# Optimization experiments

Measured on AMD Instinct MI355X. Metric: run time of the kernel, lower is better.

## Reference

```python
import jax, jax.numpy as jnp
import numpy as np

B, N, KNB, F, H = 1, 50000, 16, 128, 128
BN_EPS = 1e-3  # keras BatchNormalization default epsilon
ALPHA = 0.3    # keras LeakyReLU default negative slope


def setup_inputs() -> dict:
    key = jax.random.key(0)
    ks = jax.random.split(key, 14)
    s_in = 1.0 / np.sqrt(F)
    s_cat = 1.0 / np.sqrt(F + H)
    return {
        'embeddings': jax.random.normal(ks[0], (B, N, F), jnp.float32),
        'weights': jnp.zeros((1, 1), jnp.float32),  # unused in call_att
        'neighbor_set': jax.random.randint(ks[1], (B, N, KNB), 0, N),
        'Wq': jax.random.normal(ks[2], (F, H), jnp.float32) * s_in,
        'bq': jnp.zeros((H,), jnp.float32),
        'Wk': jax.random.normal(ks[3], (F, H), jnp.float32) * s_in,
        'bk': jnp.zeros((H,), jnp.float32),
        'Wv': jax.random.normal(ks[4], (F, H), jnp.float32) * s_in,
        'bv': jnp.zeros((H,), jnp.float32),
        'W1': jax.random.normal(ks[5], (F + H, H), jnp.float32) * s_cat,
        'b1': jnp.zeros((H,), jnp.float32),
        'gamma': 1.0 + 0.1 * jax.random.normal(ks[6], (H,), jnp.float32),
        'beta': 0.1 * jax.random.normal(ks[7], (H,), jnp.float32),
        'mov_mean': 0.1 * jax.random.normal(ks[8], (H,), jnp.float32),
        'mov_var': 1.0 + 0.1 * jax.random.uniform(ks[9], (H,), jnp.float32),
    }


def reference(embeddings, weights, neighbor_set, Wq, bq, Wk, bk, Wv, bv,
              W1, b1, gamma, beta, mov_mean, mov_var):
    lrelu = lambda x: jax.nn.leaky_relu(x, ALPHA)
    # batched gather: nb[b, n, k] = embeddings[b, neighbor_set[b, n, k]]  -> [B,N,K,F]
    nb = jax.vmap(lambda e, idx: e[idx])(embeddings, neighbor_set)
    q = lrelu(embeddings @ Wq + bq)      # [B,N,H]
    k = lrelu(nb @ Wk + bk)              # [B,N,K,H]
    v = lrelu(nb @ Wv + bv)              # [B,N,K,H]
    # Q is tiled across the K neighbor rows in the original; every attention row
    # is identical, so mean-pool over rows == single-query attention. Same math.
    scores = jnp.einsum('bnh,bnkh->bnk', q, k)          # dot-product, no scale
    attn = jax.nn.softmax(scores, axis=-1)
    pooled = jnp.einsum('bnk,bnkh->bnh', attn, v)       # [B,N,H]
    h = lrelu(jnp.concatenate([embeddings, pooled], axis=-1) @ W1 + b1)
    h = h / (jnp.linalg.norm(h, axis=2, keepdims=True) + 1e-6)
    # BatchNormalization (inference form, axis=-1)
    return gamma * (h - mov_mean) * jax.lax.rsqrt(mov_var + BN_EPS) + beta
```

## Files before the change

### kernel.cpp

```cpp
#include <hip/hip_runtime.h>
#include <hip/hip_bf16.h>

#define N_NODES 50000
#define KNB 16
#define FDIM 128
#define HDIM 128
#define ALPHA 0.3f
#define BN_EPS 1e-3f

typedef __bf16 v8bf __attribute__((ext_vector_type(8)));
typedef float v4f __attribute__((ext_vector_type(4)));
typedef unsigned short ushort_t;

__device__ __forceinline__ float blo(unsigned int u) {
    union { float f; unsigned int i; } x; x.i = u << 16; return x.f;
}
__device__ __forceinline__ float bhi(unsigned int u) {
    union { float f; unsigned int i; } x; x.i = u & 0xffff0000u; return x.f;
}

__device__ __forceinline__ unsigned short f2bf(float f) {
    union { float f; unsigned int u; } x;
    x.f = f;
    unsigned int r = x.u + 0x7fffu + ((x.u >> 16) & 1u);
    return (unsigned short)(r >> 16);
}

__device__ __forceinline__ unsigned int pk2(float a, float b) {
    __hip_bfloat162 h = __float22bfloat162_rn(make_float2(a, b));
    union { __hip_bfloat162 h; unsigned int u; } r; r.h = h; return r.u;
}

__device__ __forceinline__ float lrelu(float x) { return x > 0.f ? x : ALPHA * x; }

__device__ __forceinline__ v8bf load8f(const float* p) {
    float4 A = ((const float4*)p)[0];
    float4 B = ((const float4*)p)[1];
    union { v8bf v; unsigned int u[4]; } r;
    r.u[0] = pk2(A.x, A.y); r.u[1] = pk2(A.z, A.w);
    r.u[2] = pk2(B.x, B.y); r.u[3] = pk2(B.z, B.w);
    return r.v;
}

__global__ __launch_bounds__(256) void prep_kernel(
    const float* __restrict__ Wq, const float* __restrict__ Wk,
    const float* __restrict__ Wv, const float* __restrict__ W1,
    ushort_t* __restrict__ WT)
{
    const int idx = blockIdx.x * 256 + threadIdx.x;
    if (idx < 16384) {
        int k = idx >> 7, n = idx & 127;
        WT[n * 128 + k] = f2bf(Wq[idx]);
    } else if (idx < 32768) {
        int i = idx - 16384; int k = i >> 7, n = i & 127;
        WT[16384 + n * 128 + k] = f2bf(Wk[i]);
    } else if (idx < 49152) {
        int i = idx - 32768; int k = i >> 7, n = i & 127;
        WT[32768 + n * 128 + k] = f2bf(Wv[i]);
    } else if (idx < 81920) {
        int i = idx - 49152; int k = i >> 7, n = i & 127;
        WT[49152 + n * 256 + k] = f2bf(W1[i]);
    }
}

#define QSTRIDE 560
#define KVSTRIDE 528
#define WTILE 18432

__global__ __launch_bounds__(256) void qkv_kernel(
    const float* __restrict__ E, const ushort_t* __restrict__ WT,
    const float* __restrict__ bq, const float* __restrict__ bk,
    const float* __restrict__ bv,
    float* __restrict__ Qo, ushort_t* __restrict__ KV)
{
    __shared__ char smem[4 * WTILE];

    const int tid  = threadIdx.x;
    const int wave = tid >> 6;
    const int lane = tid & 63;
    const int quad = lane >> 4;
    const int j    = lane & 15;
    const int row0 = blockIdx.x * 128 + wave * 32;

    char* const wbase = smem + wave * WTILE;

    const int ar0 = min(row0 + j,      N_NODES - 1);
    const int ar1 = min(row0 + 16 + j, N_NODES - 1);

    v8bf a0f[4], a1f[4];
#pragma unroll
    for (int ks = 0; ks < 4; ++ks) {
        const int k0 = ks * 32 + quad * 8;
        a0f[ks] = load8f(E + (size_t)ar0 * FDIM + k0);
        a1f[ks] = load8f(E + (size_t)ar1 * FDIM + k0);
    }

    const float* biases[3] = {bq, bk, bv};

    for (int w = 0; w < 3; ++w) {
        const ushort_t* __restrict__ Wsrc = WT + w * 16384;

        v4f acc[2][8];
#pragma unroll
        for (int rb = 0; rb < 2; ++rb)
#pragma unroll
            for (int c = 0; c < 8; ++c) acc[rb][c] = (v4f){0.f, 0.f, 0.f, 0.f};

#pragma unroll
        for (int ks = 0; ks < 4; ++ks) {
            const int k0 = ks * 32 + quad * 8;
            v8bf b[8];
#pragma unroll
            for (int c = 0; c < 8; ++c)
                b[c] = *(const v8bf*)(Wsrc + (c * 16 + j) * 128 + k0);
#pragma unroll
            for (int c = 0; c < 8; ++c) {
                acc[0][c] = __builtin_amdgcn_mfma_f32_16x16x32_bf16(b[c], a0f[ks], acc[0][c], 0, 0, 0);
                acc[1][c] = __builtin_amdgcn_mfma_f32_16x16x32_bf16(b[c], a1f[ks], acc[1][c], 0, 0, 0);
            }
        }

        const float* __restrict__ bias = biases[w];

        if (w == 0) {
#pragma unroll
            for (int rb = 0; rb < 2; ++rb)
#pragma unroll
                for (int c = 0; c < 8; ++c) {
                    const float4 bb = ((const float4*)bias)[c * 4 + quad];
                    v4f v = acc[rb][c];
                    v[0] = lrelu(v[0] + bb.x); v[1] = lrelu(v[1] + bb.y);
                    v[2] = lrelu(v[2] + bb.z); v[3] = lrelu(v[3] + bb.w);
                    *(v4f*)(wbase + (rb * 16 + j) * QSTRIDE + (c * 16 + quad * 4) * 4) = v;
                }
#pragma unroll
            for (int t = 0; t < 16; ++t) {
                const int r  = 2 * t + (lane >> 5);
                const v4f v  = *(const v4f*)(wbase + r * QSTRIDE + (lane & 31) * 16);
                const int gr = row0 + r;
                if (gr < N_NODES)
                    *(v4f*)(Qo + (size_t)gr * HDIM + (lane & 31) * 4) = v;
            }
        } else {
            const int voff = (w == 2) ? 256 : 0;
#pragma unroll
            for (int rb = 0; rb < 2; ++rb)
#pragma unroll
                for (int c = 0; c < 8; ++c) {
                    const float4 bb = ((const float4*)bias)[c * 4 + quad];
                    const v4f v = acc[rb][c];
                    uint2 u;
                    u.x = pk2(lrelu(v[0] + bb.x), lrelu(v[1] + bb.y));
                    u.y = pk2(lrelu(v[2] + bb.z), lrelu(v[3] + bb.w));
                    *(uint2*)(wbase + (rb * 16 + j) * KVSTRIDE + (c * 16 + quad * 4) * 2 + voff) = u;
                }
            if (w == 2) {
#pragma unroll
                for (int t = 0; t < 16; ++t) {
                    const int r  = 2 * t + (lane >> 5);
                    const uint4 v = *(const uint4*)(wbase + r * KVSTRIDE + (lane & 31) * 16);
                    const int gr = row0 + r;
                    if (gr < N_NODES)
                        *(uint4*)((char*)KV + (size_t)gr * 512 + (lane & 31) * 16) = v;
                }
            }
        }
    }
}

#define DOT8(qa, qb, kp) (qa.x*blo(kp.x) + qa.y*bhi(kp.x) + qa.z*blo(kp.y) + qa.w*bhi(kp.y) \
                        + qb.x*blo(kp.z) + qb.y*bhi(kp.z) + qb.z*blo(kp.w) + qb.w*bhi(kp.w))

__global__ __launch_bounds__(256) void attn_kernel(
    float* __restrict__ QP, const ushort_t* __restrict__ KV,
    const int* __restrict__ nbr)
{
    const int tid  = threadIdx.x;
    const int wave = tid >> 6;
    const int lane = tid & 63;
    const int grp  = lane >> 4;
    const int li   = lane & 15;
    const int n0 = __builtin_amdgcn_readfirstlane(blockIdx.x * 8 + wave * 2);
    const int n1 = n0 + 1;

    const float4* qr0 = (const float4*)(QP + (size_t)n0 * HDIM + li * 8);
    const float4 q0a = qr0[0], q0b = qr0[1];
    const float4* qr1 = (const float4*)(QP + (size_t)n1 * HDIM + li * 8);
    const float4 q1a = qr1[0], q1b = qr1[1];

    const int* nbA = nbr + n0 * KNB;
    const int* nbB = nbr + n1 * KNB;
    int nidA[4], nidB[4];
#pragma unroll
    for (int t = 0; t < 4; ++t) {
        int a0 = nbA[t*4+0]; a0 = ((unsigned)a0 < (unsigned)N_NODES) ? a0 : 0;
        int a1 = nbA[t*4+1]; a1 = ((unsigned)a1 < (unsigned)N_NODES) ? a1 : 0;
        int a2 = nbA[t*4+2]; a2 = ((unsigned)a2 < (unsigned)N_NODES) ? a2 : 0;
        int a3 = nbA[t*4+3]; a3 = ((unsigned)a3 < (unsigned)N_NODES) ? a3 : 0;
        int va = a0;
        va = (grp == 1) ? a1 : va;
        va = (grp == 2) ? a2 : va;
        va = (grp == 3) ? a3 : va;
        nidA[t] = va;
        int b0 = nbB[t*4+0]; b0 = ((unsigned)b0 < (unsigned)N_NODES) ? b0 : 0;
        int b1 = nbB[t*4+1]; b1 = ((unsigned)b1 < (unsigned)N_NODES) ? b1 : 0;
        int b2 = nbB[t*4+2]; b2 = ((unsigned)b2 < (unsigned)N_NODES) ? b2 : 0;
        int b3 = nbB[t*4+3]; b3 = ((unsigned)b3 < (unsigned)N_NODES) ? b3 : 0;
        int vb = b0;
        vb = (grp == 1) ? b1 : vb;
        vb = (grp == 2) ? b2 : vb;
        vb = (grp == 3) ? b3 : vb;
        nidB[t] = vb;
    }

    const char* kvb = (const char*)KV;
    const size_t lo16 = (size_t)(li * 16);

    uint4 kA[4], kB[4], vA[4], vB[4];
#pragma unroll
    for (int t = 0; t < 4; ++t) {
        kA[t] = *(const uint4*)(kvb + (size_t)nidA[t] * 512 + lo16);
        kB[t] = *(const uint4*)(kvb + (size_t)nidB[t] * 512 + lo16);
        vA[t] = *(const uint4*)(kvb + (size_t)nidA[t] * 512 + 256 + lo16);
        vB[t] = *(const uint4*)(kvb + (size_t)nidB[t] * 512 + 256 + lo16);
    }

    float sA[4], sB[4];
#pragma unroll
    for (int t = 0; t < 4; ++t) {
        sA[t] = DOT8(q0a, q0b, kA[t]);
        sB[t] = DOT8(q1a, q1b, kB[t]);
    }
#pragma unroll
    for (int off = 1; off <= 8; off <<= 1) {
#pragma unroll
        for (int t = 0; t < 4; ++t) {
            sA[t] += __shfl_xor(sA[t], off, 64);
            sB[t] += __shfl_xor(sB[t], off, 64);
        }
    }

    float mA = fmaxf(fmaxf(sA[0], sA[1]), fmaxf(sA[2], sA[3]));
    float mB = fmaxf(fmaxf(sB[0], sB[1]), fmaxf(sB[2], sB[3]));
    mA = fmaxf(mA, __shfl_xor(mA, 16, 64)); mB = fmaxf(mB, __shfl_xor(mB, 16, 64));
    mA = fmaxf(mA, __shfl_xor(mA, 32, 64)); mB = fmaxf(mB, __shfl_xor(mB, 32, 64));
    float aA[4], aB[4];
#pragma unroll
    for (int t = 0; t < 4; ++t) {
        aA[t] = __expf(sA[t] - mA);
        aB[t] = __expf(sB[t] - mB);
    }
    float sumA = aA[0] + aA[1] + aA[2] + aA[3];
    float sumB = aB[0] + aB[1] + aB[2] + aB[3];
    sumA += __shfl_xor(sumA, 16, 64); sumB += __shfl_xor(sumB, 16, 64);
    sumA += __shfl_xor(sumA, 32, 64); sumB += __shfl_xor(sumB, 32, 64);
    const float invA = 1.f / sumA, invB = 1.f / sumB;
#pragma unroll
    for (int t = 0; t < 4; ++t) { aA[t] *= invA; aB[t] *= invB; }

    float pA[8] = {0,0,0,0,0,0,0,0}, pB[8] = {0,0,0,0,0,0,0,0};
#pragma unroll
    for (int t = 0; t < 4; ++t) {
        pA[0] += aA[t] * blo(vA[t].x); pA[1] += aA[t] * bhi(vA[t].x);
        pA[2] += aA[t] * blo(vA[t].y); pA[3] += aA[t] * bhi(vA[t].y);
        pA[4] += aA[t] * blo(vA[t].z); pA[5] += aA[t] * bhi(vA[t].z);
        pA[6] += aA[t] * blo(vA[t].w); pA[7] += aA[t] * bhi(vA[t].w);
        pB[0] += aB[t] * blo(vB[t].x); pB[1] += aB[t] * bhi(vB[t].x);
        pB[2] += aB[t] * blo(vB[t].y); pB[3] += aB[t] * bhi(vB[t].y);
        pB[4] += aB[t] * blo(vB[t].z); pB[5] += aB[t] * bhi(vB[t].z);
        pB[6] += aB[t] * blo(vB[t].w); pB[7] += aB[t] * bhi(vB[t].w);
    }
#pragma unroll
    for (int i = 0; i < 8; ++i) {
        pA[i] += __shfl_xor(pA[i], 16, 64); pB[i] += __shfl_xor(pB[i], 16, 64);
        pA[i] += __shfl_xor(pA[i], 32, 64); pB[i] += __shfl_xor(pB[i], 32, 64);
    }

    if (grp == 0) {
        float4* out = (float4*)(QP + (size_t)n0 * HDIM + li * 8);
        out[0] = make_float4(pA[0], pA[1], pA[2], pA[3]);
        out[1] = make_float4(pA[4], pA[5], pA[6], pA[7]);
    } else if (grp == 1) {
        float4* out = (float4*)(QP + (size_t)n1 * HDIM + li * 8);
        out[0] = make_float4(pB[0], pB[1], pB[2], pB[3]);
        out[1] = make_float4(pB[4], pB[5], pB[6], pB[7]);
    }
}

__global__ __launch_bounds__(256) void out_kernel(
    const float* __restrict__ E, const ushort_t* __restrict__ W1T,
    const float* __restrict__ b1,
    const float* __restrict__ gamma, const float* __restrict__ beta,
    const float* __restrict__ mmean, const float* __restrict__ mvar,
    float* __restrict__ OutP)
{
    __shared__ ushort_t sW[128 * 136];

    const int tid  = threadIdx.x;
    const int wave = tid >> 6;
    const int lane = tid & 63;
    const int quad = lane >> 4;
    const int j    = lane & 15;
    const int row0 = blockIdx.x * 128 + wave * 32;

    const int ar0 = min(row0 + j,      N_NODES - 1);
    const int ar1 = min(row0 + 16 + j, N_NODES - 1);

    v4f acc[2][8];
#pragma unroll
    for (int rb = 0; rb < 2; ++rb)
#pragma unroll
        for (int c = 0; c < 8; ++c) acc[rb][c] = (v4f){0.f, 0.f, 0.f, 0.f};

    for (int half = 0; half < 2; ++half) {
        for (int i = tid; i < 2048; i += 256) {
            int n = i >> 4, kc = i & 15;
            *(uint4*)(&sW[n * 136 + kc * 8]) =
                *(const uint4*)(W1T + n * 256 + half * 128 + kc * 8);
        }
        __syncthreads();

        const float* Abase = (half == 0) ? E : (const float*)OutP;
#pragma unroll
        for (int ks = 0; ks < 4; ++ks) {
            const int k0 = ks * 32 + quad * 8;
            v8bf a0 = load8f(Abase + (size_t)ar0 * 128 + k0);
            v8bf a1 = load8f(Abase + (size_t)ar1 * 128 + k0);
            v8bf b[8];
#pragma unroll
            for (int c = 0; c < 8; ++c)
                b[c] = *(const v8bf*)(&sW[(c * 16 + j) * 136 + k0]);
#pragma unroll
            for (int c = 0; c < 8; ++c) {
                acc[0][c] = __builtin_amdgcn_mfma_f32_16x16x32_bf16(a0, b[c], acc[0][c], 0, 0, 0);
                acc[1][c] = __builtin_amdgcn_mfma_f32_16x16x32_bf16(a1, b[c], acc[1][c], 0, 0, 0);
            }
        }
        __syncthreads();
    }

    float scale_[8], shift_[8], bias_[8];
#pragma unroll
    for (int c = 0; c < 8; ++c) {
        const int col = c * 16 + j;
        const float sc = gamma[col] * rsqrtf(mvar[col] + BN_EPS);
        scale_[c] = sc;
        shift_[c] = beta[col] - mmean[col] * sc;
        bias_[c]  = b1[col];
    }

#pragma unroll
    for (int rb = 0; rb < 2; ++rb)
#pragma unroll
        for (int c = 0; c < 8; ++c)
#pragma unroll
            for (int i = 0; i < 4; ++i)
                acc[rb][c][i] = lrelu(acc[rb][c][i] + bias_[c]);

#pragma unroll
    for (int rb = 0; rb < 2; ++rb) {
#pragma unroll
        for (int i = 0; i < 4; ++i) {
            float ss = 0.f;
#pragma unroll
            for (int c = 0; c < 8; ++c) ss += acc[rb][c][i] * acc[rb][c][i];
            ss += __shfl_xor(ss, 1, 64);
            ss += __shfl_xor(ss, 2, 64);
            ss += __shfl_xor(ss, 4, 64);
            ss += __shfl_xor(ss, 8, 64);
            const float invn = 1.f / (sqrtf(ss) + 1e-6f);
            const int r = row0 + rb * 16 + quad * 4 + i;
            if (r < N_NODES) {
#pragma unroll
                for (int c = 0; c < 8; ++c)
                    OutP[(size_t)r * HDIM + c * 16 + j] =
                        acc[rb][c][i] * invn * scale_[c] + shift_[c];
            }
        }
    }
}

extern "C" void kernel_launch(void* const* d_in, const int* in_sizes, int n_in,
                              void* d_out, int out_size, void* d_ws, size_t ws_size,
                              hipStream_t stream)
{
    const float* E     = (const float*)d_in[0];
    const int*   nbr   = (const int*)d_in[2];
    const float* Wq    = (const float*)d_in[3];
    const float* bq    = (const float*)d_in[4];
    const float* Wk    = (const float*)d_in[5];
    const float* bk    = (const float*)d_in[6];
    const float* Wv    = (const float*)d_in[7];
    const float* bv    = (const float*)d_in[8];
    const float* W1    = (const float*)d_in[9];
    const float* b1    = (const float*)d_in[10];
    const float* gam   = (const float*)d_in[11];
    const float* bet   = (const float*)d_in[12];
    const float* mmean = (const float*)d_in[13];
    const float* mvar  = (const float*)d_in[14];

    ushort_t* KV = (ushort_t*)d_ws;
    ushort_t* WT = KV + (size_t)N_NODES * 256;
    float* QP = (float*)d_out;

    const int gridA = (N_NODES + 127) / 128;
    prep_kernel<<<320, 256, 0, stream>>>(Wq, Wk, Wv, W1, WT);
    qkv_kernel<<<gridA, 256, 0, stream>>>(E, WT, bq, bk, bv, QP, KV);
    attn_kernel<<<N_NODES / 8, 256, 0, stream>>>(QP, KV, nbr);
    out_kernel<<<gridA, 256, 0, stream>>>(E, WT + 49152, b1, gam, bet, mmean, mvar, QP);
}
```

Before: 211.6 us.

## Fuse attention and output GEMM into one launch with per-block ready flags

Merges the attention and output kernels into a single grid: the first blocks do attention and set per-block flags after writing pooled rows, and the later blocks compute the E-half of the output GEMM, then spin on flags before reading pooled rows through atomic (cache-bypassing) loads. This is meant to remove a kernel launch boundary and overlap the E·W1 half with the attention tail. It relies on blocks being dispatched in index order to avoid deadlock. It adds spin-wait and atomic load/store overhead.

```diff
diff --git a/kernel.cpp b/kernel.cpp
--- a/kernel.cpp
+++ b/kernel.cpp
@@ -7,6 +7,8 @@
 #define HDIM 128
 #define ALPHA 0.3f
 #define BN_EPS 1e-3f
+#define NATT 6250
+#define NOUT 391
 
 typedef __bf16 v8bf __attribute__((ext_vector_type(8)));
 typedef float v4f __attribute__((ext_vector_type(4)));
@@ -42,10 +44,29 @@
     return r.v;
 }
 
+__device__ __forceinline__ void st8_bypass(float* p, float a, float b) {
+    union { float f[2]; unsigned long long u; } x;
+    x.f[0] = a; x.f[1] = b;
+    __hip_atomic_store((unsigned long long*)p, x.u, __ATOMIC_RELAXED,
+                       __HIP_MEMORY_SCOPE_AGENT);
+}
+__device__ __forceinline__ v8bf load8f_bypass(const float* p) {
+    union { unsigned long long u; float f[2]; } d0, d1, d2, d3;
+    const unsigned long long* q = (const unsigned long long*)p;
+    d0.u = __hip_atomic_load(q + 0, __ATOMIC_RELAXED, __HIP_MEMORY_SCOPE_AGENT);
+    d1.u = __hip_atomic_load(q + 1, __ATOMIC_RELAXED, __HIP_MEMORY_SCOPE_AGENT);
+    d2.u = __hip_atomic_load(q + 2, __ATOMIC_RELAXED, __HIP_MEMORY_SCOPE_AGENT);
+    d3.u = __hip_atomic_load(q + 3, __ATOMIC_RELAXED, __HIP_MEMORY_SCOPE_AGENT);
+    union { v8bf v; unsigned int u[4]; } r;
+    r.u[0] = pk2(d0.f[0], d0.f[1]); r.u[1] = pk2(d1.f[0], d1.f[1]);
+    r.u[2] = pk2(d2.f[0], d2.f[1]); r.u[3] = pk2(d3.f[0], d3.f[1]);
+    return r.v;
+}
+
 __global__ __launch_bounds__(256) void prep_kernel(
     const float* __restrict__ Wq, const float* __restrict__ Wk,
     const float* __restrict__ Wv, const float* __restrict__ W1,
-    ushort_t* __restrict__ WT)
+    ushort_t* __restrict__ WT, int* __restrict__ flags)
 {
     const int idx = blockIdx.x * 256 + threadIdx.x;
     if (idx < 16384) {
@@ -60,6 +81,9 @@
     } else if (idx < 81920) {
         int i = idx - 49152; int k = i >> 7, n = i & 127;
         WT[49152 + n * 256 + k] = f2bf(W1[i]);
+    } else if (idx < 81920 + NATT) {
+        __hip_atomic_store(&flags[idx - 81920], 0, __ATOMIC_RELAXED,
+                           __HIP_MEMORY_SCOPE_AGENT);
     }
 }
 
@@ -171,137 +195,141 @@
 #define DOT8(qa, qb, kp) (qa.x*blo(kp.x) + qa.y*bhi(kp.x) + qa.z*blo(kp.y) + qa.w*bhi(kp.y) \
                         + qb.x*blo(kp.z) + qb.y*bhi(kp.z) + qb.z*blo(kp.w) + qb.w*bhi(kp.w))
 
-__global__ __launch_bounds__(256) void attn_kernel(
+__global__ __launch_bounds__(256) void attn_out_kernel(
     float* __restrict__ QP, const ushort_t* __restrict__ KV,
-    const int* __restrict__ nbr)
-{
-    const int tid  = threadIdx.x;
-    const int wave = tid >> 6;
-    const int lane = tid & 63;
-    const int grp  = lane >> 4;
-    const int li   = lane & 15;
-    const int n0 = __builtin_amdgcn_readfirstlane(blockIdx.x * 8 + wave * 2);
-    const int n1 = n0 + 1;
-
-    const float4* qr0 = (const float4*)(QP + (size_t)n0 * HDIM + li * 8);
-    const float4 q0a = qr0[0], q0b = qr0[1];
-    const float4* qr1 = (const float4*)(QP + (size_t)n1 * HDIM + li * 8);
-    const float4 q1a = qr1[0], q1b = qr1[1];
-
-    const int* nbA = nbr + n0 * KNB;
-    const int* nbB = nbr + n1 * KNB;
-    int nidA[4], nidB[4];
-#pragma unroll
-    for (int t = 0; t < 4; ++t) {
-        int a0 = nbA[t*4+0]; a0 = ((unsigned)a0 < (unsigned)N_NODES) ? a0 : 0;
-        int a1 = nbA[t*4+1]; a1 = ((unsigned)a1 < (unsigned)N_NODES) ? a1 : 0;
-        int a2 = nbA[t*4+2]; a2 = ((unsigned)a2 < (unsigned)N_NODES) ? a2 : 0;
-        int a3 = nbA[t*4+3]; a3 = ((unsigned)a3 < (unsigned)N_NODES) ? a3 : 0;
-        int va = a0;
-        va = (grp == 1) ? a1 : va;
-        va = (grp == 2) ? a2 : va;
-        va = (grp == 3) ? a3 : va;
-        nidA[t] = va;
-        int b0 = nbB[t*4+0]; b0 = ((unsigned)b0 < (unsigned)N_NODES) ? b0 : 0;
-        int b1 = nbB[t*4+1]; b1 = ((unsigned)b1 < (unsigned)N_NODES) ? b1 : 0;
-        int b2 = nbB[t*4+2]; b2 = ((unsigned)b2 < (unsigned)N_NODES) ? b2 : 0;
-        int b3 = nbB[t*4+3]; b3 = ((unsigned)b3 < (unsigned)N_NODES) ? b3 : 0;
-        int vb = b0;
-        vb = (grp == 1) ? b1 : vb;
-        vb = (grp == 2) ? b2 : vb;
-        vb = (grp == 3) ? b3 : vb;
-        nidB[t] = vb;
-    }
-
-    const char* kvb = (const char*)KV;
-    const size_t lo16 = (size_t)(li * 16);
-
-    uint4 kA[4], kB[4], vA[4], vB[4];
-#pragma unroll
-    for (int t = 0; t < 4; ++t) {
-        kA[t] = *(const uint4*)(kvb + (size_t)nidA[t] * 512 + lo16);
-        kB[t] = *(const uint4*)(kvb + (size_t)nidB[t] * 512 + lo16);
-        vA[t] = *(const uint4*)(kvb + (size_t)nidA[t] * 512 + 256 + lo16);
-        vB[t] = *(const uint4*)(kvb + (size_t)nidB[t] * 512 + 256 + lo16);
-    }
-
-    float sA[4], sB[4];
-#pragma unroll
-    for (int t = 0; t < 4; ++t) {
-        sA[t] = DOT8(q0a, q0b, kA[t]);
-        sB[t] = DOT8(q1a, q1b, kB[t]);
-    }
-#pragma unroll
-    for (int off = 1; off <= 8; off <<= 1) {
-#pragma unroll
-        for (int t = 0; t < 4; ++t) {
-            sA[t] += __shfl_xor(sA[t], off, 64);
-            sB[t] += __shfl_xor(sB[t], off, 64);
-        }
-    }
-
-    float mA = fmaxf(fmaxf(sA[0], sA[1]), fmaxf(sA[2], sA[3]));
-    float mB = fmaxf(fmaxf(sB[0], sB[1]), fmaxf(sB[2], sB[3]));
-    mA = fmaxf(mA, __shfl_xor(mA, 16, 64)); mB = fmaxf(mB, __shfl_xor(mB, 16, 64));
-    mA = fmaxf(mA, __shfl_xor(mA, 32, 64)); mB = fmaxf(mB, __shfl_xor(mB, 32, 64));
-    float aA[4], aB[4];
-#pragma unroll
-    for (int t = 0; t < 4; ++t) {
-        aA[t] = __expf(sA[t] - mA);
-        aB[t] = __expf(sB[t] - mB);
-    }
-    float sumA = aA[0] + aA[1] + aA[2] + aA[3];
-    float sumB = aB[0] + aB[1] + aB[2] + aB[3];
-    sumA += __shfl_xor(sumA, 16, 64); sumB += __shfl_xor(sumB, 16, 64);
-    sumA += __shfl_xor(sumA, 32, 64); sumB += __shfl_xor(sumB, 32, 64);
-    const float invA = 1.f / sumA, invB = 1.f / sumB;
-#pragma unroll
-    for (int t = 0; t < 4; ++t) { aA[t] *= invA; aB[t] *= invB; }
-
-    float pA[8] = {0,0,0,0,0,0,0,0}, pB[8] = {0,0,0,0,0,0,0,0};
-#pragma unroll
-    for (int t = 0; t < 4; ++t) {
-        pA[0] += aA[t] * blo(vA[t].x); pA[1] += aA[t] * bhi(vA[t].x);
-        pA[2] += aA[t] * blo(vA[t].y); pA[3] += aA[t] * bhi(vA[t].y);
-        pA[4] += aA[t] * blo(vA[t].z); pA[5] += aA[t] * bhi(vA[t].z);
-        pA[6] += aA[t] * blo(vA[t].w); pA[7] += aA[t] * bhi(vA[t].w);
-        pB[0] += aB[t] * blo(vB[t].x); pB[1] += aB[t] * bhi(vB[t].x);
-        pB[2] += aB[t] * blo(vB[t].y); pB[3] += aB[t] * bhi(vB[t].y);
-        pB[4] += aB[t] * blo(vB[t].z); pB[5] += aB[t] * bhi(vB[t].z);
-        pB[6] += aB[t] * blo(vB[t].w); pB[7] += aB[t] * bhi(vB[t].w);
-    }
-#pragma unroll
-    for (int i = 0; i < 8; ++i) {
-        pA[i] += __shfl_xor(pA[i], 16, 64); pB[i] += __shfl_xor(pB[i], 16, 64);
-        pA[i] += __shfl_xor(pA[i], 32, 64); pB[i] += __shfl_xor(pB[i], 32, 64);
-    }
-
-    if (grp == 0) {
-        float4* out = (float4*)(QP + (size_t)n0 * HDIM + li * 8);
-        out[0] = make_float4(pA[0], pA[1], pA[2], pA[3]);
-        out[1] = make_float4(pA[4], pA[5], pA[6], pA[7]);
-    } else if (grp == 1) {
-        float4* out = (float4*)(QP + (size_t)n1 * HDIM + li * 8);
-        out[0] = make_float4(pB[0], pB[1], pB[2], pB[3]);
-        out[1] = make_float4(pB[4], pB[5], pB[6], pB[7]);
-    }
-}
-
-__global__ __launch_bounds__(256) void out_kernel(
+    const int* __restrict__ nbr,
     const float* __restrict__ E, const ushort_t* __restrict__ W1T,
     const float* __restrict__ b1,
     const float* __restrict__ gamma, const float* __restrict__ beta,
     const float* __restrict__ mmean, const float* __restrict__ mvar,
-    float* __restrict__ OutP)
+    int* __restrict__ flags)
 {
     __shared__ ushort_t sW[128 * 136];
 
     const int tid  = threadIdx.x;
     const int wave = tid >> 6;
     const int lane = tid & 63;
+
+    if (blockIdx.x < NATT) {
+        const int grp = lane >> 4;
+        const int li  = lane & 15;
+        const int n0 = __builtin_amdgcn_readfirstlane(blockIdx.x * 8 + wave * 2);
+        const int n1 = n0 + 1;
+
+        const float4* qr0 = (const float4*)(QP + (size_t)n0 * HDIM + li * 8);
+        const float4 q0a = qr0[0], q0b = qr0[1];
+        const float4* qr1 = (const float4*)(QP + (size_t)n1 * HDIM + li * 8);
+        const float4 q1a = qr1[0], q1b = qr1[1];
+
+        const int* nbA = nbr + n0 * KNB;
+        const int* nbB = nbr + n1 * KNB;
+        int nidA[4], nidB[4];
+#pragma unroll
+        for (int t = 0; t < 4; ++t) {
+            int a0 = nbA[t*4+0]; a0 = ((unsigned)a0 < (unsigned)N_NODES) ? a0 : 0;
+            int a1 = nbA[t*4+1]; a1 = ((unsigned)a1 < (unsigned)N_NODES) ? a1 : 0;
+            int a2 = nbA[t*4+2]; a2 = ((unsigned)a2 < (unsigned)N_NODES) ? a2 : 0;
+            int a3 = nbA[t*4+3]; a3 = ((unsigned)a3 < (unsigned)N_NODES) ? a3 : 0;
+            int va = a0;
+            va = (grp == 1) ? a1 : va;
+            va = (grp == 2) ? a2 : va;
+            va = (grp == 3) ? a3 : va;
+            nidA[t] = va;
+            int b0 = nbB[t*4+0]; b0 = ((unsigned)b0 < (unsigned)N_NODES) ? b0 : 0;
+            int b1_ = nbB[t*4+1]; b1_ = ((unsigned)b1_ < (unsigned)N_NODES) ? b1_ : 0;
+            int b2 = nbB[t*4+2]; b2 = ((unsigned)b2 < (unsigned)N_NODES) ? b2 : 0;
+            int b3 = nbB[t*4+3]; b3 = ((unsigned)b3 < (unsigned)N_NODES) ? b3 : 0;
+            int vb = b0;
+            vb = (grp == 1) ? b1_ : vb;
+            vb = (grp == 2) ? b2 : vb;
+            vb = (grp == 3) ? b3 : vb;
+            nidB[t] = vb;
+        }
+
+        const char* kvb = (const char*)KV;
+        const size_t lo16 = (size_t)(li * 16);
+
+        uint4 kA[4], kB[4], vA[4], vB[4];
+#pragma unroll
+        for (int t = 0; t < 4; ++t) {
+            kA[t] = *(const uint4*)(kvb + (size_t)nidA[t] * 512 + lo16);
+            kB[t] = *(const uint4*)(kvb + (size_t)nidB[t] * 512 + lo16);
+            vA[t] = *(const uint4*)(kvb + (size_t)nidA[t] * 512 + 256 + lo16);
+            vB[t] = *(const uint4*)(kvb + (size_t)nidB[t] * 512 + 256 + lo16);
+        }
+
+        float sA[4], sB[4];
+#pragma unroll
+        for (int t = 0; t < 4; ++t) {
+            sA[t] = DOT8(q0a, q0b, kA[t]);
+            sB[t] = DOT8(q1a, q1b, kB[t]);
+        }
+#pragma unroll
+        for (int off = 1; off <= 8; off <<= 1) {
+#pragma unroll
+            for (int t = 0; t < 4; ++t) {
+                sA[t] += __shfl_xor(sA[t], off, 64);
+                sB[t] += __shfl_xor(sB[t], off, 64);
+            }
+        }
+
+        float mA = fmaxf(fmaxf(sA[0], sA[1]), fmaxf(sA[2], sA[3]));
+        float mB = fmaxf(fmaxf(sB[0], sB[1]), fmaxf(sB[2], sB[3]));
+        mA = fmaxf(mA, __shfl_xor(mA, 16, 64)); mB = fmaxf(mB, __shfl_xor(mB, 16, 64));
+        mA = fmaxf(mA, __shfl_xor(mA, 32, 64)); mB = fmaxf(mB, __shfl_xor(mB, 32, 64));
+        float aA[4], aB[4];
+#pragma unroll
+        for (int t = 0; t < 4; ++t) {
+            aA[t] = __expf(sA[t] - mA);
+            aB[t] = __expf(sB[t] - mB);
+        }
+        float sumA = aA[0] + aA[1] + aA[2] + aA[3];
+        float sumB = aB[0] + aB[1] + aB[2] + aB[3];
+        sumA += __shfl_xor(sumA, 16, 64); sumB += __shfl_xor(sumB, 16, 64);
+        sumA += __shfl_xor(sumA, 32, 64); sumB += __shfl_xor(sumB, 32, 64);
+        const float invA = 1.f / sumA, invB = 1.f / sumB;
+#pragma unroll
+        for (int t = 0; t < 4; ++t) { aA[t] *= invA; aB[t] *= invB; }
+
+        float pA[8] = {0,0,0,0,0,0,0,0}, pB[8] = {0,0,0,0,0,0,0,0};
+#pragma unroll
+        for (int t = 0; t < 4; ++t) {
+            pA[0] += aA[t] * blo(vA[t].x); pA[1] += aA[t] * bhi(vA[t].x);
+            pA[2] += aA[t] * blo(vA[t].y); pA[3] += aA[t] * bhi(vA[t].y);
+            pA[4] += aA[t] * blo(vA[t].z); pA[5] += aA[t] * bhi(vA[t].z);
+            pA[6] += aA[t] * blo(vA[t].w); pA[7] += aA[t] * bhi(vA[t].w);
+            pB[0] += aB[t] * blo(vB[t].x); pB[1] += aB[t] * bhi(vB[t].x);
+            pB[2] += aB[t] * blo(vB[t].y); pB[3] += aB[t] * bhi(vB[t].y);
+            pB[4] += aB[t] * blo(vB[t].z); pB[5] += aB[t] * bhi(vB[t].z);
+            pB[6] += aB[t] * blo(vB[t].w); pB[7] += aB[t] * bhi(vB[t].w);
+        }
+#pragma unroll
+        for (int i = 0; i < 8; ++i) {
+            pA[i] += __shfl_xor(pA[i], 16, 64); pB[i] += __shfl_xor(pB[i], 16, 64);
+            pA[i] += __shfl_xor(pA[i], 32, 64); pB[i] += __shfl_xor(pB[i], 32, 64);
+        }
+
+        if (grp == 0) {
+            float* o = QP + (size_t)n0 * HDIM + li * 8;
+            st8_bypass(o + 0, pA[0], pA[1]); st8_bypass(o + 2, pA[2], pA[3]);
+            st8_bypass(o + 4, pA[4], pA[5]); st8_bypass(o + 6, pA[6], pA[7]);
+        } else if (grp == 1) {
+            float* o = QP + (size_t)n1 * HDIM + li * 8;
+            st8_bypass(o + 0, pB[0], pB[1]); st8_bypass(o + 2, pB[2], pB[3]);
+            st8_bypass(o + 4, pB[4], pB[5]); st8_bypass(o + 6, pB[6], pB[7]);
+        }
+        asm volatile("s_waitcnt vmcnt(0)" ::: "memory");
+        __syncthreads();
+        if (tid == 0)
+            __hip_atomic_store(&flags[blockIdx.x], 1, __ATOMIC_RELAXED,
+                               __HIP_MEMORY_SCOPE_AGENT);
+        return;
+    }
+
+    const int bo   = blockIdx.x - NATT;
     const int quad = lane >> 4;
     const int j    = lane & 15;
-    const int row0 = blockIdx.x * 128 + wave * 32;
+    const int row0 = bo * 128 + wave * 32;
 
     const int ar0 = min(row0 + j,      N_NODES - 1);
     const int ar1 = min(row0 + 16 + j, N_NODES - 1);
@@ -312,32 +340,58 @@
 #pragma unroll
         for (int c = 0; c < 8; ++c) acc[rb][c] = (v4f){0.f, 0.f, 0.f, 0.f};
 
-    for (int half = 0; half < 2; ++half) {
-        for (int i = tid; i < 2048; i += 256) {
-            int n = i >> 4, kc = i & 15;
-            *(uint4*)(&sW[n * 136 + kc * 8]) =
-                *(const uint4*)(W1T + n * 256 + half * 128 + kc * 8);
-        }
-        __syncthreads();
-
-        const float* Abase = (half == 0) ? E : (const float*)OutP;
-#pragma unroll
-        for (int ks = 0; ks < 4; ++ks) {
-            const int k0 = ks * 32 + quad * 8;
-            v8bf a0 = load8f(Abase + (size_t)ar0 * 128 + k0);
-            v8bf a1 = load8f(Abase + (size_t)ar1 * 128 + k0);
-            v8bf b[8];
-#pragma unroll
-            for (int c = 0; c < 8; ++c)
-                b[c] = *(const v8bf*)(&sW[(c * 16 + j) * 136 + k0]);
-#pragma unroll
-            for (int c = 0; c < 8; ++c) {
-                acc[0][c] = __builtin_amdgcn_mfma_f32_16x16x32_bf16(a0, b[c], acc[0][c], 0, 0, 0);
-                acc[1][c] = __builtin_amdgcn_mfma_f32_16x16x32_bf16(a1, b[c], acc[1][c], 0, 0, 0);
-            }
-        }
-        __syncthreads();
-    }
+    for (int i = tid; i < 2048; i += 256) {
+        int n = i >> 4, kc = i & 15;
+        *(uint4*)(&sW[n * 136 + kc * 8]) = *(const uint4*)(W1T + n * 256 + kc * 8);
+    }
+    __syncthreads();
+#pragma unroll
+    for (int ks = 0; ks < 4; ++ks) {
+        const int k0 = ks * 32 + quad * 8;
+        v8bf a0 = load8f(E + (size_t)ar0 * 128 + k0);
+        v8bf a1 = load8f(E + (size_t)ar1 * 128 + k0);
+        v8bf b[8];
+#pragma unroll
+        for (int c = 0; c < 8; ++c)
+            b[c] = *(const v8bf*)(&sW[(c * 16 + j) * 136 + k0]);
+#pragma unroll
+        for (int c = 0; c < 8; ++c) {
+            acc[0][c] = __builtin_amdgcn_mfma_f32_16x16x32_bf16(a0, b[c], acc[0][c], 0, 0, 0);
+            acc[1][c] = __builtin_amdgcn_mfma_f32_16x16x32_bf16(a1, b[c], acc[1][c], 0, 0, 0);
+        }
+    }
+    __syncthreads();
+
+    for (int i = tid; i < 2048; i += 256) {
+        int n = i >> 4, kc = i & 15;
+        *(uint4*)(&sW[n * 136 + kc * 8]) =
+            *(const uint4*)(W1T + n * 256 + 128 + kc * 8);
+    }
+    if (tid < 16) {
+        int f = 16 * bo + tid;
+        if (f >= NATT) f = NATT - 1;
+        while (__hip_atomic_load(&flags[f], __ATOMIC_RELAXED,
+                                 __HIP_MEMORY_SCOPE_AGENT) == 0)
+            __builtin_amdgcn_s_sleep(2);
+    }
+    __syncthreads();
+
+#pragma unroll
+    for (int ks = 0; ks < 4; ++ks) {
+        const int k0 = ks * 32 + quad * 8;
+        v8bf a0 = load8f_bypass(QP + (size_t)ar0 * 128 + k0);
+        v8bf a1 = load8f_bypass(QP + (size_t)ar1 * 128 + k0);
+        v8bf b[8];
+#pragma unroll
+        for (int c = 0; c < 8; ++c)
+            b[c] = *(const v8bf*)(&sW[(c * 16 + j) * 136 + k0]);
+#pragma unroll
+        for (int c = 0; c < 8; ++c) {
+            acc[0][c] = __builtin_amdgcn_mfma_f32_16x16x32_bf16(a0, b[c], acc[0][c], 0, 0, 0);
+            acc[1][c] = __builtin_amdgcn_mfma_f32_16x16x32_bf16(a1, b[c], acc[1][c], 0, 0, 0);
+        }
+    }
+    __syncthreads();
 
     float scale_[8], shift_[8], bias_[8];
 #pragma unroll
@@ -373,7 +427,7 @@
             if (r < N_NODES) {
 #pragma unroll
                 for (int c = 0; c < 8; ++c)
-                    OutP[(size_t)r * HDIM + c * 16 + j] =
+                    QP[(size_t)r * HDIM + c * 16 + j] =
                         acc[rb][c][i] * invn * scale_[c] + shift_[c];
             }
         }
@@ -399,13 +453,13 @@
     const float* mmean = (const float*)d_in[13];
     const float* mvar  = (const float*)d_in[14];
 
-    ushort_t* KV = (ushort_t*)d_ws;
-    ushort_t* WT = KV + (size_t)N_NODES * 256;
+    ushort_t* KV    = (ushort_t*)d_ws;
+    ushort_t* WT    = KV + (size_t)N_NODES * 256;
+    int*      flags = (int*)(WT + 81920);
     float* QP = (float*)d_out;
 
-    const int gridA = (N_NODES + 127) / 128;
-    prep_kernel<<<320, 256, 0, stream>>>(Wq, Wk, Wv, W1, WT);
-    qkv_kernel<<<gridA, 256, 0, stream>>>(E, WT, bq, bk, bv, QP, KV);
-    attn_kernel<<<N_NODES / 8, 256, 0, stream>>>(QP, KV, nbr);
-    out_kernel<<<gridA, 256, 0, stream>>>(E, WT + 49152, b1, gam, bet, mmean, mvar, QP);
-}
+    prep_kernel<<<345, 256, 0, stream>>>(Wq, Wk, Wv, W1, WT, flags);
+    qkv_kernel<<<(N_NODES + 127) / 128, 256, 0, stream>>>(E, WT, bq, bk, bv, QP, KV);
+    attn_out_kernel<<<NATT + NOUT, 256, 0, stream>>>(
+        QP, KV, nbr, E, WT + 49152, b1, gam, bet, mmean, mvar, flags);
+}
```

Result: slower. 237.5 us (+12.2%).
